# Kernel optimization log

Measured on AMD Instinct MI355X. Metric: run time of the kernel, lower is better.

Reference implementation:

```python
import jax, jax.numpy as jnp
import numpy as np

B, C, W, H = 4, 256, 64, 64

def setup_inputs() -> dict:
    key = jax.random.key(0)
    ks = jax.random.split(key, 6)
    return {
        "fm_source": jax.random.normal(ks[0], (B, C, W, H), dtype=jnp.float32),
        "fm_reference": jax.random.normal(ks[1], (B, C, W, H), dtype=jnp.float32),
        "w_lambda": jax.random.normal(ks[2], (1, C, 1, 1), dtype=jnp.float32) * 0.05,
        "b_lambda": jax.random.normal(ks[3], (1,), dtype=jnp.float32) * 0.05,
        "w_beta": jax.random.normal(ks[4], (1, C, 1, 1), dtype=jnp.float32) * 0.05,
        "b_beta": jax.random.normal(ks[5], (1,), dtype=jnp.float32) * 0.05,
    }

def reference(fm_source, fm_reference, w_lambda, b_lambda, w_beta, b_beta):
    b, c, w, h = fm_reference.shape
    n = w * h
    # 1x1 convs on the reference feature map -> per-pixel scalars, flattened to [B, N]
    wl = w_lambda.reshape(c)
    wb = w_beta.reshape(c)
    ref_flat = fm_reference.reshape(b, c, n)   # [B, C, N]
    src_flat = fm_source.reshape(b, c, n)      # [B, C, N]
    old_lambda = jnp.einsum("bcn,c->bn", ref_flat, wl) + b_lambda[0]  # [B, N]
    old_beta = jnp.einsum("bcn,c->bn", ref_flat, wb) + b_beta[0]      # [B, N]
    # energy[b, i, j] = <src pixel i, ref pixel j> over channels
    energy = jnp.einsum("bci,bcj->bij", src_flat, ref_flat)  # [B, N, N]
    attention = jax.nn.softmax(energy, axis=-1)              # softmax over ref pixels j
    # new_lambda[b, i] = sum_j old_lambda[b, j] * attention[b, i, j]
    new_lambda = jnp.einsum("bj,bij->bi", old_lambda, attention).reshape(b, 1, w, h)
    new_beta = jnp.einsum("bj,bij->bi", old_beta, attention).reshape(b, 1, w, h)
    # broadcast modulation over the 256 channels
    return new_lambda * fm_source + new_beta
```

## Files before the change

### kernel.cpp

```cpp
#include <hip/hip_runtime.h>


#define B_ 4
#define C_ 256
#define N_ 4096
#define LOG2E 1.44269504f
#define SHIFT2 86.5617f
#define JSLICE 16
#define BN_ (B_ * N_)
#define NT_ 8

typedef _Float16 half_t;
typedef _Float16 v8h  __attribute__((ext_vector_type(8)));
typedef float    v16f __attribute__((ext_vector_type(16)));

#define GLDS16(g, l) __builtin_amdgcn_global_load_lds(                         \
    (const __attribute__((address_space(1))) void*)(g),                        \
    (__attribute__((address_space(3))) void*)(l), 16, 0, 0)

__global__ void k_prep(const float* __restrict__ src,
                       const float* __restrict__ ref,
                       const float* __restrict__ wl, const float* __restrict__ bl,
                       const float* __restrict__ wb, const float* __restrict__ bb,
                       half_t* __restrict__ s16, half_t* __restrict__ r16,
                       float* __restrict__ oldL, float* __restrict__ oldB) {
    if (blockIdx.z == 8) {
        int b  = blockIdx.y;
        int n0 = blockIdx.x * 64;
        int nl = threadIdx.x & 63;
        int cq = threadIdx.x >> 6;
        const float* p = ref + ((size_t)b * C_ + cq * 64) * N_ + n0 + nl;
        float aL = 0.f, aB = 0.f;
#pragma unroll 8
        for (int c = 0; c < 64; c++) {
            float v = p[(size_t)c * N_];
            aL += v * wl[cq * 64 + c];
            aB += v * wb[cq * 64 + c];
        }
        __shared__ float red[8][64];
        red[cq][nl]     = aL;
        red[4 + cq][nl] = aB;
        __syncthreads();
        if (threadIdx.x < 64) {
            int t = threadIdx.x;
            oldL[(size_t)b * N_ + n0 + t] =
                red[0][t] + red[1][t] + red[2][t] + red[3][t] + bl[0];
        } else if (threadIdx.x < 128) {
            int t = threadIdx.x - 64;
            oldB[(size_t)b * N_ + n0 + t] =
                red[4][t] + red[5][t] + red[6][t] + red[7][t] + bb[0];
        }
        return;
    }
    __shared__ float tile[64][65];
    int z  = blockIdx.z;
    int b  = z & 3;
    const float* in  = (z < B_) ? src : ref;
    half_t*      out = (z < B_) ? s16 : r16;
    float scale      = (z < B_) ? LOG2E : 1.0f;
    int c0 = blockIdx.y * 64;
    int n0 = blockIdx.x * 64;
    int tx = threadIdx.x & 15, ty = threadIdx.x >> 4;
#pragma unroll
    for (int q = 0; q < 4; q++) {
        int c = ty + q * 16;
        float4 v = *(const float4*)(in + ((size_t)b * C_ + c0 + c) * N_ + n0 + tx * 4);
        tile[c][tx * 4 + 0] = v.x;
        tile[c][tx * 4 + 1] = v.y;
        tile[c][tx * 4 + 2] = v.z;
        tile[c][tx * 4 + 3] = v.w;
    }
    __syncthreads();
    int r   = threadIdx.x & 31;
    int lhi = (threadIdx.x >> 5) & 1;
    int wv  = threadIdx.x >> 6;
#pragma unroll
    for (int nt = 0; nt < 2; nt++) {
        int nl = nt * 32 + r;
        v8h o;
#pragma unroll
        for (int e = 0; e < 8; e++)
            o[e] = (half_t)(tile[wv * 16 + lhi * 8 + e][nl] * scale);
        size_t tj = (size_t)(n0 >> 5) + nt;
        size_t kb = (size_t)(c0 >> 4) + wv;
        *(v8h*)(out + ((((size_t)b * 128 + tj) * 16 + kb) * 64 + (threadIdx.x & 63)) * 8) = o;
    }
}

__global__ __launch_bounds__(256, 2) void k_flash(
        const half_t* __restrict__ sT, const half_t* __restrict__ rT,
        const float* __restrict__ oldL, const float* __restrict__ oldB,
        float* __restrict__ part ) {
    __shared__ half_t lds[2][8192];
    int bid    = blockIdx.x;
    int b      = bid & 3;
    int jslice = (bid >> 2) & (JSLICE - 1);
    int itile  = bid >> 6;
    int tid    = threadIdx.x;
    int wv     = tid >> 6;
    int lane   = tid & 63;
    int l31    = lane & 31, lhi = lane >> 5;
    int ti     = itile * 4 + wv;
    int i0     = ti * 32;
    int j0     = jslice * (N_ / JSLICE);
    int tj0    = j0 >> 5;

    const half_t* aP = sT + (((size_t)b * 128 + ti) * 16) * 512 + (size_t)lane * 8;
    v8h a[16];
#pragma unroll
    for (int kb = 0; kb < 16; kb++) a[kb] = *(const v8h*)(aP + (size_t)kb * 512);

    const half_t* bBase = rT + (((size_t)b * 128 + tj0) * 16) * 512;
    const float*  oLp = oldL + (size_t)b * N_ + j0 + l31;
    const float*  oBp = oldB + (size_t)b * N_ + j0 + l31;

    float sp[16], sl[16], sb[16];
#pragma unroll
    for (int r = 0; r < 16; r++) { sp[r] = 0.f; sl[r] = 0.f; sb[r] = 0.f; }

#pragma unroll
    for (int q = 0; q < 4; q++) {
        int chunk = q * 4 + wv;
        GLDS16(bBase + (size_t)chunk * 512 + (size_t)lane * 8,
               &lds[0][(size_t)chunk * 512]);
    }

    for (int jt = 0; jt < NT_; jt++) {
        __syncthreads();
        if (jt + 1 < NT_) {
            const half_t* g = bBase + (size_t)(jt + 1) * 8192;
#pragma unroll
            for (int q = 0; q < 4; q++) {
                int chunk = q * 4 + wv;
                GLDS16(g + (size_t)chunk * 512 + (size_t)lane * 8,
                       &lds[(jt + 1) & 1][(size_t)chunk * 512]);
            }
        }
        const half_t* bt = lds[jt & 1] + (size_t)lane * 8;
        v16f acc;
#pragma unroll
        for (int r = 0; r < 16; r++) acc[r] = -SHIFT2;
#pragma unroll
        for (int kb = 0; kb < 16; kb++) {
            v8h bf = *(const v8h*)(bt + (size_t)kb * 512);
            acc = __builtin_amdgcn_mfma_f32_32x32x16_f16(a[kb], bf, acc, 0, 0, 0);
        }
        float lam = oLp[jt * 32], bet = oBp[jt * 32];
#pragma unroll
        for (int r = 0; r < 16; r++) {
            float p = __builtin_amdgcn_exp2f(acc[r]);
            sp[r] += p;
            sl[r] += p * lam;
            sb[r] += p * bet;
        }
    }

    float* pSP = part + ((size_t)jslice * 3 + 0) * BN_;
    float* pSL = part + ((size_t)jslice * 3 + 1) * BN_;
    float* pSB = part + ((size_t)jslice * 3 + 2) * BN_;
#pragma unroll
    for (int r = 0; r < 16; r++) {
        float tp = sp[r], tl = sl[r], tb = sb[r];
#pragma unroll
        for (int m = 1; m <= 16; m <<= 1) {
            tp += __shfl_xor(tp, m, 64);
            tl += __shfl_xor(tl, m, 64);
            tb += __shfl_xor(tb, m, 64);
        }
        if (l31 == 0) {
            int row = (r & 3) + 8 * (r >> 2) + 4 * lhi;
            size_t ig = (size_t)b * N_ + i0 + row;
            pSP[ig] = tp; pSL[ig] = tl; pSB[ig] = tb;
        }
    }
}

__global__ void k_post(const float* __restrict__ src,
                       const float* __restrict__ part,
                       float* __restrict__ out) {
    __shared__ float sL[256], sB[256];
    int b  = blockIdx.x;
    int n0 = blockIdx.y * 256;
    int c0 = blockIdx.z * 64;
    int t  = threadIdx.x;
    size_t bn = (size_t)b * N_ + n0 + t;
    float sp = 0.f, sl = 0.f, sb = 0.f;
#pragma unroll
    for (int s = 0; s < JSLICE; s++) {
        sp += part[((size_t)s * 3 + 0) * BN_ + bn];
        sl += part[((size_t)s * 3 + 1) * BN_ + bn];
        sb += part[((size_t)s * 3 + 2) * BN_ + bn];
    }
    float inv = 1.0f / sp;
    sL[t] = sl * inv;
    sB[t] = sb * inv;
    __syncthreads();
    const float* sp0 = src + ((size_t)b * C_ + c0) * N_ + n0;
    float*       op0 = out + ((size_t)b * C_ + c0) * N_ + n0;
#pragma unroll 4
    for (int c = 0; c < 64; c++) {
        float v = sp0[(size_t)c * N_ + t];
        op0[(size_t)c * N_ + t] = sL[t] * v + sB[t];
    }
}

extern "C" void kernel_launch(void* const* d_in, const int* in_sizes, int n_in,
                              void* d_out, int out_size, void* d_ws, size_t ws_size,
                              hipStream_t stream) {
    const float* src = (const float*)d_in[0];
    const float* ref = (const float*)d_in[1];
    const float* wl  = (const float*)d_in[2];
    const float* bl  = (const float*)d_in[3];
    const float* wb  = (const float*)d_in[4];
    const float* bb  = (const float*)d_in[5];
    float* out = (float*)d_out;

    float* oldL = (float*)d_ws;
    float* oldB = oldL + BN_;
    float* part = oldB + BN_;
    size_t needF  = ((size_t)2 + 3 * JSLICE) * BN_ * sizeof(float);
    size_t need16 = (size_t)2 * B_ * N_ * C_ * sizeof(half_t);
    half_t* s16;
    if (ws_size >= needF + need16) s16 = (half_t*)((char*)d_ws + needF);
    else                           s16 = (half_t*)d_out;
    half_t* r16 = s16 + (size_t)B_ * N_ * C_;

    k_prep<<<dim3(N_ / 64, C_ / 64, 9), 256, 0, stream>>>(
        src, ref, wl, bl, wb, bb, s16, r16, oldL, oldB);
    k_flash<<<2048, 256, 0, stream>>>(s16, r16, oldL, oldB, part);
    k_post<<<dim3(B_, N_ / 256, C_ / 64), 256, 0, stream>>>(src, part, out);
}
```

Before: 148.6 us.

## Widen flash blocks to eight waves, halve j-slices, vectorize prep and post

The attention kernel now runs 512-thread blocks in which eight waves share each staged reference tile in LDS, instead of four. The j dimension is split into 8 slices of 16 tiles rather than 16 slices of 8. This cuts global-to-LDS traffic per i-row and halves the partial-sum buffer written and then re-read. The prep kernel is retiled to 16 channels by 256 pixels, and the post kernel reduces partials and applies the modulation with float4 loads and stores. The trade-offs are fewer, larger flash blocks, so the 512-block grid gives each CU only about two blocks and less latency hiding, and higher register pressure under the new launch bounds.

```diff
diff --git a/kernel.cpp b/kernel.cpp
--- a/kernel.cpp
+++ b/kernel.cpp
@@ -6,9 +6,9 @@
 #define N_ 4096
 #define LOG2E 1.44269504f
 #define SHIFT2 86.5617f
-#define JSLICE 16
+#define JSLICE 8
 #define BN_ (B_ * N_)
-#define NT_ 8
+#define NT_ 16
 
 typedef _Float16 half_t;
 typedef _Float16 v8h  __attribute__((ext_vector_type(8)));
@@ -25,8 +25,9 @@
                        half_t* __restrict__ s16, half_t* __restrict__ r16,
                        float* __restrict__ oldL, float* __restrict__ oldB) {
     if (blockIdx.z == 8) {
-        int b  = blockIdx.y;
-        int n0 = blockIdx.x * 64;
+        int flat = blockIdx.y * 16 + blockIdx.x;
+        int b  = flat & 3;
+        int n0 = (flat >> 2) * 64;
         int nl = threadIdx.x & 63;
         int cq = threadIdx.x >> 6;
         const float* p = ref + ((size_t)b * C_ + cq * 64) * N_ + n0 + nl;
@@ -52,42 +53,42 @@
         }
         return;
     }
-    __shared__ float tile[64][65];
+    __shared__ float tile[16][257];
     int z  = blockIdx.z;
     int b  = z & 3;
     const float* in  = (z < B_) ? src : ref;
     half_t*      out = (z < B_) ? s16 : r16;
     float scale      = (z < B_) ? LOG2E : 1.0f;
-    int c0 = blockIdx.y * 64;
-    int n0 = blockIdx.x * 64;
-    int tx = threadIdx.x & 15, ty = threadIdx.x >> 4;
-#pragma unroll
-    for (int q = 0; q < 4; q++) {
-        int c = ty + q * 16;
-        float4 v = *(const float4*)(in + ((size_t)b * C_ + c0 + c) * N_ + n0 + tx * 4);
-        tile[c][tx * 4 + 0] = v.x;
-        tile[c][tx * 4 + 1] = v.y;
-        tile[c][tx * 4 + 2] = v.z;
-        tile[c][tx * 4 + 3] = v.w;
+    int n0 = blockIdx.x * 256;
+    int c0 = blockIdx.y * 16;
+    int t    = threadIdx.x;
+    int lane = t & 63;
+    int wvid = t >> 6;
+#pragma unroll
+    for (int p = 0; p < 4; p++) {
+        int c = p * 4 + wvid;
+        float4 v = *(const float4*)(in + ((size_t)b * C_ + c0 + c) * N_ + n0 + lane * 4);
+        tile[c][lane * 4 + 0] = v.x;
+        tile[c][lane * 4 + 1] = v.y;
+        tile[c][lane * 4 + 2] = v.z;
+        tile[c][lane * 4 + 3] = v.w;
     }
     __syncthreads();
-    int r   = threadIdx.x & 31;
-    int lhi = (threadIdx.x >> 5) & 1;
-    int wv  = threadIdx.x >> 6;
-#pragma unroll
-    for (int nt = 0; nt < 2; nt++) {
-        int nl = nt * 32 + r;
+    int l31 = lane & 31, lhi = lane >> 5;
+    size_t kb = (size_t)(c0 >> 4);
+#pragma unroll
+    for (int p = 0; p < 2; p++) {
+        int tjl = p * 4 + wvid;
         v8h o;
 #pragma unroll
         for (int e = 0; e < 8; e++)
-            o[e] = (half_t)(tile[wv * 16 + lhi * 8 + e][nl] * scale);
-        size_t tj = (size_t)(n0 >> 5) + nt;
-        size_t kb = (size_t)(c0 >> 4) + wv;
-        *(v8h*)(out + ((((size_t)b * 128 + tj) * 16 + kb) * 64 + (threadIdx.x & 63)) * 8) = o;
-    }
-}
-
-__global__ __launch_bounds__(256, 2) void k_flash(
+            o[e] = (half_t)(tile[lhi * 8 + e][tjl * 32 + l31] * scale);
+        size_t tj = (size_t)(n0 >> 5) + tjl;
+        *(v8h*)(out + ((((size_t)b * 128 + tj) * 16 + kb) * 64 + lane) * 8) = o;
+    }
+}
+
+__global__ __launch_bounds__(512, 2) void k_flash(
         const half_t* __restrict__ sT, const half_t* __restrict__ rT,
         const float* __restrict__ oldL, const float* __restrict__ oldB,
         float* __restrict__ part ) {
@@ -95,12 +96,12 @@
     int bid    = blockIdx.x;
     int b      = bid & 3;
     int jslice = (bid >> 2) & (JSLICE - 1);
-    int itile  = bid >> 6;
+    int iblock = bid >> 5;
     int tid    = threadIdx.x;
     int wv     = tid >> 6;
     int lane   = tid & 63;
     int l31    = lane & 31, lhi = lane >> 5;
-    int ti     = itile * 4 + wv;
+    int ti     = iblock * 8 + wv;
     int i0     = ti * 32;
     int j0     = jslice * (N_ / JSLICE);
     int tj0    = j0 >> 5;
@@ -119,8 +120,8 @@
     for (int r = 0; r < 16; r++) { sp[r] = 0.f; sl[r] = 0.f; sb[r] = 0.f; }
 
 #pragma unroll
-    for (int q = 0; q < 4; q++) {
-        int chunk = q * 4 + wv;
+    for (int q = 0; q < 2; q++) {
+        int chunk = q * 8 + wv;
         GLDS16(bBase + (size_t)chunk * 512 + (size_t)lane * 8,
                &lds[0][(size_t)chunk * 512]);
     }
@@ -130,8 +131,8 @@
         if (jt + 1 < NT_) {
             const half_t* g = bBase + (size_t)(jt + 1) * 8192;
 #pragma unroll
-            for (int q = 0; q < 4; q++) {
-                int chunk = q * 4 + wv;
+            for (int q = 0; q < 2; q++) {
+                int chunk = q * 8 + wv;
                 GLDS16(g + (size_t)chunk * 512 + (size_t)lane * 8,
                        &lds[(jt + 1) & 1][(size_t)chunk * 512]);
             }
@@ -178,29 +179,35 @@
 __global__ void k_post(const float* __restrict__ src,
                        const float* __restrict__ part,
                        float* __restrict__ out) {
-    __shared__ float sL[256], sB[256];
     int b  = blockIdx.x;
-    int n0 = blockIdx.y * 256;
-    int c0 = blockIdx.z * 64;
+    int n0 = blockIdx.y * 1024;
+    int c0 = blockIdx.z * 16;
     int t  = threadIdx.x;
-    size_t bn = (size_t)b * N_ + n0 + t;
-    float sp = 0.f, sl = 0.f, sb = 0.f;
+    size_t bn = (size_t)b * N_ + n0 + t * 4;
+    float4 sp = {0.f, 0.f, 0.f, 0.f}, sl = sp, sb = sp;
 #pragma unroll
     for (int s = 0; s < JSLICE; s++) {
-        sp += part[((size_t)s * 3 + 0) * BN_ + bn];
-        sl += part[((size_t)s * 3 + 1) * BN_ + bn];
-        sb += part[((size_t)s * 3 + 2) * BN_ + bn];
-    }
-    float inv = 1.0f / sp;
-    sL[t] = sl * inv;
-    sB[t] = sb * inv;
-    __syncthreads();
-    const float* sp0 = src + ((size_t)b * C_ + c0) * N_ + n0;
-    float*       op0 = out + ((size_t)b * C_ + c0) * N_ + n0;
+        float4 p0 = *(const float4*)(part + ((size_t)s * 3 + 0) * BN_ + bn);
+        float4 p1 = *(const float4*)(part + ((size_t)s * 3 + 1) * BN_ + bn);
+        float4 p2 = *(const float4*)(part + ((size_t)s * 3 + 2) * BN_ + bn);
+        sp.x += p0.x; sp.y += p0.y; sp.z += p0.z; sp.w += p0.w;
+        sl.x += p1.x; sl.y += p1.y; sl.z += p1.z; sl.w += p1.w;
+        sb.x += p2.x; sb.y += p2.y; sb.z += p2.z; sb.w += p2.w;
+    }
+    float4 L, T;
+    L.x = sl.x / sp.x; L.y = sl.y / sp.y; L.z = sl.z / sp.z; L.w = sl.w / sp.w;
+    T.x = sb.x / sp.x; T.y = sb.y / sp.y; T.z = sb.z / sp.z; T.w = sb.w / sp.w;
+    const float* sp0 = src + ((size_t)b * C_ + c0) * N_ + n0 + t * 4;
+    float*       op0 = out + ((size_t)b * C_ + c0) * N_ + n0 + t * 4;
 #pragma unroll 4
-    for (int c = 0; c < 64; c++) {
-        float v = sp0[(size_t)c * N_ + t];
-        op0[(size_t)c * N_ + t] = sL[t] * v + sB[t];
+    for (int c = 0; c < 16; c++) {
+        float4 v = *(const float4*)(sp0 + (size_t)c * N_);
+        float4 o;
+        o.x = L.x * v.x + T.x;
+        o.y = L.y * v.y + T.y;
+        o.z = L.z * v.z + T.z;
+        o.w = L.w * v.w + T.w;
+        *(float4*)(op0 + (size_t)c * N_) = o;
     }
 }
 
@@ -225,8 +232,8 @@
     else                           s16 = (half_t*)d_out;
     half_t* r16 = s16 + (size_t)B_ * N_ * C_;
 
-    k_prep<<<dim3(N_ / 64, C_ / 64, 9), 256, 0, stream>>>(
+    k_prep<<<dim3(N_ / 256, C_ / 16, 9), 256, 0, stream>>>(
         src, ref, wl, bl, wb, bb, s16, r16, oldL, oldB);
-    k_flash<<<2048, 256, 0, stream>>>(s16, r16, oldL, oldB, part);
-    k_post<<<dim3(B_, N_ / 256, C_ / 64), 256, 0, stream>>>(src, part, out);
-}
+    k_flash<<<512, 512, 0, stream>>>(s16, r16, oldL, oldB, part);
+    k_post<<<dim3(B_, N_ / 1024, C_ / 16), 256, 0, stream>>>(src, part, out);
+}
```

Measured after the change: 146.8 us. Within noise of the previous version (-1.2%).
